# Performance work log

Hardware: AMD Instinct MI355X
Metric: run time of the kernel (lower is better)

## Reference

```python
import jax, jax.numpy as jnp
import numpy as np

N_NODES = 50000
N_EDGES = 1600000
IN_DIM = 128
HID = 128


def setup_inputs() -> dict:
    key = jax.random.key(0)
    ks = jax.random.split(key, 12)
    s = 1.0 / np.sqrt(HID)
    return {
        "x": jax.random.normal(ks[0], (N_NODES, IN_DIM), jnp.float32),
        "src": jax.random.randint(ks[1], (N_EDGES,), 0, N_NODES, jnp.int32),
        "dst": jax.random.randint(ks[2], (N_EDGES,), 0, N_NODES, jnp.int32),
        "W0": jax.random.normal(ks[3], (IN_DIM, HID), jnp.float32) * s,
        "b0": jnp.zeros((HID,), jnp.float32),
        "W1": jax.random.normal(ks[4], (HID, HID), jnp.float32) * s,
        "b1": jnp.zeros((HID,), jnp.float32),
        "W2": jax.random.normal(ks[5], (HID, HID), jnp.float32) * s,
        "b2": jnp.zeros((HID,), jnp.float32),
        "w_pg": jax.random.normal(ks[6], (HID, 1), jnp.float32) * s,
        "b_pg": jnp.zeros((1,), jnp.float32),
        "w_pd": jax.random.normal(ks[7], (HID, 1), jnp.float32) * s,
        "b_pd": jnp.zeros((1,), jnp.float32),
        "w_v": jax.random.normal(ks[8], (HID, 1), jnp.float32) * s,
        "b_v": jnp.zeros((1,), jnp.float32),
    }


def _gcn_layer(h, src, dst, W, b):
    # DGL-style GCN: gather source features along edges, sum-scatter to dst,
    # then per-node Linear + ReLU.  agg: [N, d]
    agg = jax.ops.segment_sum(h[src], dst, num_segments=N_NODES)
    return jax.nn.relu(agg @ W + b)


def reference(x, src, dst, W0, b0, W1, b1, W2, b2, w_pg, b_pg, w_pd, b_pd, w_v, b_v):
    h = _gcn_layer(x, src, dst, W0, b0)
    h = _gcn_layer(h, src, dst, W1, b1)
    h = _gcn_layer(h, src, dst, W2, b2)
    mN = jnp.mean(h, axis=0, keepdims=True)          # dgl.mean_nodes -> [1, HID]
    v = mN @ w_v + b_v                                # [1, 1]
    pi_graph = h @ w_pg + b_pg                        # [N, 1]
    pi_done = mN @ w_pd + b_pd                        # [1, 1]
    pi = jnp.concatenate([pi_graph, pi_done], axis=0)  # [N+1, 1]
    return (pi, v)
```

## Files before the change

kernel.cpp:

```cpp
#include <hip/hip_runtime.h>
#include <hip/hip_bf16.h>


#define HID 128
#define NBLK 256
#define BSH 6
#define SCAN_CHUNK 1024

typedef __attribute__((ext_vector_type(8))) short short8;
typedef __attribute__((ext_vector_type(4))) float f32x4;

__device__ __forceinline__ unsigned int f2bf(float f) {
    unsigned int u = __float_as_uint(f);
    return (u + 0x7fffu + ((u >> 16) & 1u)) >> 16;
}
__device__ __forceinline__ float bf2f(unsigned short u) {
    return __uint_as_float(((unsigned int)u) << 16);
}

__global__ __launch_bounds__(256) void f32_to_bf16_kernel(
        const float4* __restrict__ in, ushort4* __restrict__ out, int n4) {
    for (int i = blockIdx.x * blockDim.x + threadIdx.x; i < n4; i += gridDim.x * blockDim.x) {
        float4 v = in[i];
        ushort4 o;
        o.x = (unsigned short)f2bf(v.x); o.y = (unsigned short)f2bf(v.y);
        o.z = (unsigned short)f2bf(v.z); o.w = (unsigned short)f2bf(v.w);
        out[i] = o;
    }
}

__global__ __launch_bounds__(256) void pack_w3_kernel(
        const float* __restrict__ W0, const float* __restrict__ W1,
        const float* __restrict__ W2, unsigned short* __restrict__ pw) {
    for (int j = blockIdx.x * blockDim.x + threadIdx.x; j < 3 * 16384;
         j += gridDim.x * blockDim.x) {
        int jj = j & 16383, which = j >> 14;
        const float* W = (which == 0) ? W0 : (which == 1) ? W1 : W2;
        int i = jj & 7, lane = (jj >> 3) & 63, kk = (jj >> 9) & 3, c = (jj >> 11) & 7;
        int k = kk * 32 + (lane >> 4) * 8 + i;
        int col = c * 16 + (lane & 15);
        pw[j] = (unsigned short)f2bf(W[k * 128 + col]);
    }
}

__global__ __launch_bounds__(256) void bhist_kernel(const int* __restrict__ dst,
        int* __restrict__ tbl, int ne, int nb, int epb) {
    __shared__ int lcnt[1024];
    const int k = blockIdx.x, t = threadIdx.x;
    for (int b = t; b < nb; b += 256) lcnt[b] = 0;
    __syncthreads();
    const int beg = k * epb, end = min(ne, beg + epb);
    for (int j = beg + t; j < end; j += 256)
        atomicAdd(&lcnt[dst[j] >> BSH], 1);
    __syncthreads();
    for (int b = t; b < nb; b += 256) tbl[b * NBLK + k] = lcnt[b];
}

__global__ __launch_bounds__(256) void scan_p1_kernel(const int* __restrict__ tbl,
        int* __restrict__ bsum, int sz) {
    __shared__ int sh[256];
    const int g = blockIdx.x, t = threadIdx.x;
    const int base = g * SCAN_CHUNK + t * 4;
    int s = 0;
    if (base + 3 < sz) {
        int4 v = *(const int4*)(tbl + base);
        s = v.x + v.y + v.z + v.w;
    } else {
        for (int i = 0; i < 4; ++i) if (base + i < sz) s += tbl[base + i];
    }
    sh[t] = s;
    __syncthreads();
    for (int off = 128; off > 0; off >>= 1) {
        if (t < off) sh[t] += sh[t + off];
        __syncthreads();
    }
    if (t == 0) bsum[g] = sh[0];
}

__global__ __launch_bounds__(256) void scan_p2_kernel(int* __restrict__ bsum, int ng) {
    __shared__ int sh[256];
    const int t = threadIdx.x;
    int v = (t < ng) ? bsum[t] : 0;
    sh[t] = v;
    __syncthreads();
    for (int off = 1; off < 256; off <<= 1) {
        int a = sh[t];
        int b = (t >= off) ? sh[t - off] : 0;
        __syncthreads();
        sh[t] = a + b;
        __syncthreads();
    }
    if (t < ng) bsum[t] = sh[t] - v;
}

__global__ __launch_bounds__(256) void scan_p3_kernel(int* __restrict__ tbl,
        const int* __restrict__ bsum, int sz) {
    __shared__ int sh[256];
    const int g = blockIdx.x, t = threadIdx.x;
    const int base = g * SCAN_CHUNK + t * 4;
    int4 v = make_int4(0, 0, 0, 0);
    if (base + 3 < sz) {
        v = *(const int4*)(tbl + base);
    } else {
        if (base + 0 < sz) v.x = tbl[base + 0];
        if (base + 1 < sz) v.y = tbl[base + 1];
        if (base + 2 < sz) v.z = tbl[base + 2];
    }
    int s = v.x + v.y + v.z + v.w;
    sh[t] = s;
    __syncthreads();
    for (int off = 1; off < 256; off <<= 1) {
        int a = sh[t];
        int b = (t >= off) ? sh[t - off] : 0;
        __syncthreads();
        sh[t] = a + b;
        __syncthreads();
    }
    int pre = bsum[g] + sh[t] - s;
    int o0 = pre, o1 = pre + v.x, o2 = o1 + v.y, o3 = o2 + v.z;
    if (base + 3 < sz) {
        *(int4*)(tbl + base) = make_int4(o0, o1, o2, o3);
    } else {
        if (base + 0 < sz) tbl[base + 0] = o0;
        if (base + 1 < sz) tbl[base + 1] = o1;
        if (base + 2 < sz) tbl[base + 2] = o2;
    }
}

__global__ __launch_bounds__(256) void bucket_scatter_kernel(
        const int* __restrict__ src, const int* __restrict__ dst,
        const int* __restrict__ tbl, int* __restrict__ pairs,
        int ne, int nb, int epb) {
    __shared__ int cur[1024];
    const int k = blockIdx.x, t = threadIdx.x;
    for (int b = t; b < nb; b += 256) cur[b] = tbl[b * NBLK + k];
    __syncthreads();
    const int beg = k * epb, end = min(ne, beg + epb);
    for (int j = beg + t; j < end; j += 256) {
        int d = dst[j];
        int pos = atomicAdd(&cur[d >> BSH], 1);
        pairs[pos] = (src[j] << BSH) | (d & 63);
    }
}

__global__ __launch_bounds__(256) void fine_scatter_kernel(
        const int* __restrict__ pairs, const int* __restrict__ tbl,
        int* __restrict__ row_ptr, int* __restrict__ eidx,
        int ne, int nb, int n) {
    __shared__ int cnt[64], cur[64];
    const int b = blockIdx.x, t = threadIdx.x;
    const int node0 = b << BSH;
    if (t < 64) cnt[t] = 0;
    __syncthreads();
    const int beg = tbl[b * NBLK];
    const int end = (b == nb - 1) ? ne : tbl[(b + 1) * NBLK];
    for (int j = beg + t; j < end; j += 256) atomicAdd(&cnt[pairs[j] & 63], 1);
    __syncthreads();
    if (t == 0) {
        int run = beg;
        #pragma unroll
        for (int i = 0; i < 64; ++i) { cur[i] = run; run += cnt[i]; }
    }
    __syncthreads();
    if (t < 64 && node0 + t < n) row_ptr[node0 + t] = cur[t];
    if (b == nb - 1 && t == 0) row_ptr[n] = ne;
    __syncthreads();
    for (int j = beg + t; j < end; j += 256) {
        int v = pairs[j];
        int pos = atomicAdd(&cur[v & 63], 1);
        eidx[pos] = v >> BSH;
    }
}

__global__ __launch_bounds__(256) void layer_fused_kernel(
        const uint2* __restrict__ xb, const int* __restrict__ row_ptr,
        const int* __restrict__ eidx, const short* __restrict__ packw,
        const float* __restrict__ bias, unsigned short* __restrict__ hb,
        float* __restrict__ part, float* __restrict__ pig_out,
        const float* __restrict__ w_pg, const float* __restrict__ b_pg,
        int n) {
    __shared__ unsigned short Ash[64][136];
    __shared__ float colp[4][128];
    const int t = threadIdx.x;

    {
        const int grp = t >> 5, lane = t & 31;
        for (int i = 0; i < 8; ++i) {
            const int r = grp * 8 + i;
            const int g = blockIdx.x * 64 + r;
            float4 acc = make_float4(0.f, 0.f, 0.f, 0.f);
            if (g < n) {
                const int beg = row_ptr[g], end = row_ptr[g + 1];
                int e = beg;
                for (; e + 4 <= end; e += 4) {
                    int s0 = eidx[e], s1 = eidx[e + 1], s2 = eidx[e + 2], s3 = eidx[e + 3];
                    uint2 v0 = xb[(size_t)s0 * 32 + lane];
                    uint2 v1 = xb[(size_t)s1 * 32 + lane];
                    uint2 v2 = xb[(size_t)s2 * 32 + lane];
                    uint2 v3 = xb[(size_t)s3 * 32 + lane];
                    acc.x += __uint_as_float(v0.x << 16); acc.y += __uint_as_float(v0.x & 0xffff0000u);
                    acc.z += __uint_as_float(v0.y << 16); acc.w += __uint_as_float(v0.y & 0xffff0000u);
                    acc.x += __uint_as_float(v1.x << 16); acc.y += __uint_as_float(v1.x & 0xffff0000u);
                    acc.z += __uint_as_float(v1.y << 16); acc.w += __uint_as_float(v1.y & 0xffff0000u);
                    acc.x += __uint_as_float(v2.x << 16); acc.y += __uint_as_float(v2.x & 0xffff0000u);
                    acc.z += __uint_as_float(v2.y << 16); acc.w += __uint_as_float(v2.y & 0xffff0000u);
                    acc.x += __uint_as_float(v3.x << 16); acc.y += __uint_as_float(v3.x & 0xffff0000u);
                    acc.z += __uint_as_float(v3.y << 16); acc.w += __uint_as_float(v3.y & 0xffff0000u);
                }
                for (; e < end; ++e) {
                    int s = eidx[e];
                    uint2 v = xb[(size_t)s * 32 + lane];
                    acc.x += __uint_as_float(v.x << 16); acc.y += __uint_as_float(v.x & 0xffff0000u);
                    acc.z += __uint_as_float(v.y << 16); acc.w += __uint_as_float(v.y & 0xffff0000u);
                }
            }
            uint2 o;
            o.x = f2bf(acc.x) | (f2bf(acc.y) << 16);
            o.y = f2bf(acc.z) | (f2bf(acc.w) << 16);
            *(uint2*)&Ash[r][lane * 4] = o;
        }
    }
    __syncthreads();

    const int w = t >> 6, l = t & 63;
    const int m = l & 15, hi = l >> 4;
    const int row0 = blockIdx.x * 64 + w * 16;

    short8 afrag[4];
    #pragma unroll
    for (int kk = 0; kk < 4; ++kk)
        afrag[kk] = *(const short8*)&Ash[w * 16 + m][kk * 32 + hi * 8];

    f32x4 acc[8] = {};
    #pragma unroll
    for (int kk = 0; kk < 4; ++kk) {
        #pragma unroll
        for (int c = 0; c < 8; ++c) {
            short8 bfrag = *(const short8*)(packw + ((size_t)(c * 4 + kk) * 64 + l) * 8);
            acc[c] = __builtin_amdgcn_mfma_f32_16x16x32_bf16(afrag[kk], bfrag, acc[c], 0, 0, 0);
        }
    }

    float hvv[8][4];
    #pragma unroll
    for (int c = 0; c < 8; ++c) {
        float bcol = bias[c * 16 + m];
        #pragma unroll
        for (int r = 0; r < 4; ++r) {
            int row = row0 + hi * 4 + r;
            float hv = (row < n) ? fmaxf(acc[c][r] + bcol, 0.f) : 0.f;
            hvv[c][r] = hv;
            if (row < n)
                hb[(size_t)row * 128 + c * 16 + m] = (unsigned short)f2bf(hv);
        }
    }

    if (w_pg) {
        #pragma unroll
        for (int r = 0; r < 4; ++r) {
            float p = 0.f;
            #pragma unroll
            for (int c = 0; c < 8; ++c) p += hvv[c][r] * w_pg[c * 16 + m];
            #pragma unroll
            for (int off = 1; off < 16; off <<= 1) p += __shfl_xor(p, off);
            int row = row0 + hi * 4 + r;
            if (m == 0 && row < n) pig_out[row] = p + b_pg[0];
        }
        #pragma unroll
        for (int c = 0; c < 8; ++c) {
            float v = hvv[c][0] + hvv[c][1] + hvv[c][2] + hvv[c][3];
            v += __shfl_xor(v, 16);
            v += __shfl_xor(v, 32);
            if (hi == 0) colp[w][c * 16 + m] = v;
        }
        __syncthreads();
        if (t < 128)
            part[(size_t)blockIdx.x * 128 + t] =
                colp[0][t] + colp[1][t] + colp[2][t] + colp[3][t];
    }
}

__global__ __launch_bounds__(1024) void head_final_kernel(
        const float* __restrict__ part, int nparts,
        const float* __restrict__ w_v, const float* __restrict__ b_v,
        const float* __restrict__ w_pd, const float* __restrict__ b_pd,
        float* __restrict__ out, int n_nodes) {
    __shared__ float sh[32][128];
    __shared__ float sv[128], sd[128];
    const int t = threadIdx.x;
    const int d4 = t & 31, pg = t >> 5;
    float4 acc = make_float4(0.f, 0.f, 0.f, 0.f);
    for (int i = pg; i < nparts; i += 32) {
        float4 v = *(const float4*)(part + (size_t)i * 128 + d4 * 4);
        acc.x += v.x; acc.y += v.y; acc.z += v.z; acc.w += v.w;
    }
    *(float4*)&sh[pg][d4 * 4] = acc;
    __syncthreads();
    for (int off = 16; off > 0; off >>= 1) {
        if (pg < off) {
            float4 a = *(float4*)&sh[pg][d4 * 4];
            float4 b = *(float4*)&sh[pg + off][d4 * 4];
            a.x += b.x; a.y += b.y; a.z += b.z; a.w += b.w;
            *(float4*)&sh[pg][d4 * 4] = a;
        }
        __syncthreads();
    }
    if (t < 128) {
        float mm = sh[0][t] / (float)n_nodes;
        sv[t] = mm * w_v[t];
        sd[t] = mm * w_pd[t];
    }
    __syncthreads();
    for (int off = 64; off > 0; off >>= 1) {
        if (t < off) { sv[t] += sv[t + off]; sd[t] += sd[t + off]; }
        __syncthreads();
    }
    if (t == 0) {
        out[n_nodes] = sd[0] + b_pd[0];
        out[n_nodes + 1] = sv[0] + b_v[0];
    }
}

static inline size_t align_up(size_t v, size_t a) { return (v + a - 1) & ~(a - 1); }

extern "C" void kernel_launch(void* const* d_in, const int* in_sizes, int n_in,
                              void* d_out, int out_size, void* d_ws, size_t ws_size,
                              hipStream_t stream) {
    const float* x    = (const float*)d_in[0];
    const int*   src  = (const int*)d_in[1];
    const int*   dst  = (const int*)d_in[2];
    const float* W0   = (const float*)d_in[3];
    const float* b0   = (const float*)d_in[4];
    const float* W1   = (const float*)d_in[5];
    const float* b1   = (const float*)d_in[6];
    const float* W2   = (const float*)d_in[7];
    const float* b2   = (const float*)d_in[8];
    const float* w_pg = (const float*)d_in[9];
    const float* b_pg = (const float*)d_in[10];
    const float* w_pd = (const float*)d_in[11];
    const float* b_pd = (const float*)d_in[12];
    const float* w_v  = (const float*)d_in[13];
    const float* b_v  = (const float*)d_in[14];
    float* out = (float*)d_out;

    const int NN = in_sizes[0] / HID;
    const int NE = in_sizes[1];
    const int NB = (NN + 63) >> BSH;
    const int SZ = NB * NBLK;
    const int EPB = (NE + NBLK - 1) / NBLK;
    const int NG = (SZ + SCAN_CHUNK - 1) / SCAN_CHUNK;
    const int LBLK = (NN + 63) / 64;

    char* w = (char*)d_ws;
    int* tbl      = (int*)w;            w += align_up((size_t)SZ * 4, 256);
    int* bsum     = (int*)w;            w += align_up((size_t)256 * 4, 256);
    int* row_ptr  = (int*)w;            w += align_up((size_t)(NN + 1) * 4, 256);
    int* eidx     = (int*)w;            w += align_up((size_t)NE * 4, 256);
    unsigned short* xb = (unsigned short*)w; w += align_up((size_t)NN * HID * 2, 256);
    unsigned short* hb = (unsigned short*)w; w += align_up((size_t)NN * HID * 2, 256);
    unsigned short* hb2 = (unsigned short*)w; w += align_up((size_t)NN * HID * 2, 256);
    unsigned short* pw = (unsigned short*)w; w += align_up((size_t)3 * 16384 * 2, 256);
    float* part   = (float*)w;          w += align_up((size_t)LBLK * 128 * 4, 256);
    int* pairs    = (int*)hb;
    (void)ws_size; (void)n_in; (void)out_size;

    f32_to_bf16_kernel<<<2048, 256, 0, stream>>>((const float4*)x, (ushort4*)xb, NN * 32);
    pack_w3_kernel<<<48, 256, 0, stream>>>(W0, W1, W2, pw);

    bhist_kernel<<<NBLK, 256, 0, stream>>>(dst, tbl, NE, NB, EPB);
    scan_p1_kernel<<<NG, 256, 0, stream>>>(tbl, bsum, SZ);
    scan_p2_kernel<<<1, 256, 0, stream>>>(bsum, NG);
    scan_p3_kernel<<<NG, 256, 0, stream>>>(tbl, bsum, SZ);
    bucket_scatter_kernel<<<NBLK, 256, 0, stream>>>(src, dst, tbl, pairs, NE, NB, EPB);
    fine_scatter_kernel<<<NB, 256, 0, stream>>>(pairs, tbl, row_ptr, eidx, NE, NB, NN);

    layer_fused_kernel<<<LBLK, 256, 0, stream>>>(
        (const uint2*)xb, row_ptr, eidx, (const short*)pw, b0, hb2,
        nullptr, nullptr, nullptr, nullptr, NN);
    layer_fused_kernel<<<LBLK, 256, 0, stream>>>(
        (const uint2*)hb2, row_ptr, eidx, (const short*)(pw + 16384), b1, hb,
        nullptr, nullptr, nullptr, nullptr, NN);
    layer_fused_kernel<<<LBLK, 256, 0, stream>>>(
        (const uint2*)hb, row_ptr, eidx, (const short*)(pw + 32768), b2, hb2,
        part, out, w_pg, b_pg, NN);

    head_final_kernel<<<1, 1024, 0, stream>>>(part, LBLK, w_v, b_v, w_pd, b_pd, out, NN);
}
```

Measured before the change: 314.4 us.

## Split fused aggregate+GEMM layer into separate aggregation and MFMA GEMM kernels

Unfuses each GCN layer into a standalone gather/aggregate kernel, with one 32-lane group per node and an 8-way unrolled edge loop, followed by a separate MFMA GEMM kernel that reads the aggregated bf16 rows from global memory. The aim is more parallelism and memory-level parallelism in the gather, which was limited by each block serially processing 64 rows before its GEMM. The cost is an extra global write and read of the N×128 bf16 aggregate per layer and three more kernel launches. The buffers are also rearranged so aggb is reused across layers and hb is overwritten in place by the GEMM output.

```diff
diff --git a/kernel.cpp b/kernel.cpp
--- a/kernel.cpp
+++ b/kernel.cpp
@@ -172,64 +172,80 @@
     }
 }
 
-__global__ __launch_bounds__(256) void layer_fused_kernel(
+__global__ __launch_bounds__(256) void aggregate_bf_kernel(
         const uint2* __restrict__ xb, const int* __restrict__ row_ptr,
-        const int* __restrict__ eidx, const short* __restrict__ packw,
-        const float* __restrict__ bias, unsigned short* __restrict__ hb,
+        const int* __restrict__ eidx, uint2* __restrict__ aggb, int n) {
+    int g = (int)((blockIdx.x * blockDim.x + threadIdx.x) >> 5);
+    int lane = threadIdx.x & 31;
+    if (g >= n) return;
+    const int beg = row_ptr[g], end = row_ptr[g + 1];
+    float4 acc = make_float4(0.f, 0.f, 0.f, 0.f);
+    int e = beg;
+    for (; e + 8 <= end; e += 8) {
+        uint2 v0 = xb[(size_t)eidx[e + 0] * 32 + lane];
+        uint2 v1 = xb[(size_t)eidx[e + 1] * 32 + lane];
+        uint2 v2 = xb[(size_t)eidx[e + 2] * 32 + lane];
+        uint2 v3 = xb[(size_t)eidx[e + 3] * 32 + lane];
+        uint2 v4 = xb[(size_t)eidx[e + 4] * 32 + lane];
+        uint2 v5 = xb[(size_t)eidx[e + 5] * 32 + lane];
+        uint2 v6 = xb[(size_t)eidx[e + 6] * 32 + lane];
+        uint2 v7 = xb[(size_t)eidx[e + 7] * 32 + lane];
+        acc.x += __uint_as_float(v0.x << 16); acc.y += __uint_as_float(v0.x & 0xffff0000u);
+        acc.z += __uint_as_float(v0.y << 16); acc.w += __uint_as_float(v0.y & 0xffff0000u);
+        acc.x += __uint_as_float(v1.x << 16); acc.y += __uint_as_float(v1.x & 0xffff0000u);
+        acc.z += __uint_as_float(v1.y << 16); acc.w += __uint_as_float(v1.y & 0xffff0000u);
+        acc.x += __uint_as_float(v2.x << 16); acc.y += __uint_as_float(v2.x & 0xffff0000u);
+        acc.z += __uint_as_float(v2.y << 16); acc.w += __uint_as_float(v2.y & 0xffff0000u);
+        acc.x += __uint_as_float(v3.x << 16); acc.y += __uint_as_float(v3.x & 0xffff0000u);
+        acc.z += __uint_as_float(v3.y << 16); acc.w += __uint_as_float(v3.y & 0xffff0000u);
+        acc.x += __uint_as_float(v4.x << 16); acc.y += __uint_as_float(v4.x & 0xffff0000u);
+        acc.z += __uint_as_float(v4.y << 16); acc.w += __uint_as_float(v4.y & 0xffff0000u);
+        acc.x += __uint_as_float(v5.x << 16); acc.y += __uint_as_float(v5.x & 0xffff0000u);
+        acc.z += __uint_as_float(v5.y << 16); acc.w += __uint_as_float(v5.y & 0xffff0000u);
+        acc.x += __uint_as_float(v6.x << 16); acc.y += __uint_as_float(v6.x & 0xffff0000u);
+        acc.z += __uint_as_float(v6.y << 16); acc.w += __uint_as_float(v6.y & 0xffff0000u);
+        acc.x += __uint_as_float(v7.x << 16); acc.y += __uint_as_float(v7.x & 0xffff0000u);
+        acc.z += __uint_as_float(v7.y << 16); acc.w += __uint_as_float(v7.y & 0xffff0000u);
+    }
+    for (; e + 2 <= end; e += 2) {
+        uint2 v0 = xb[(size_t)eidx[e + 0] * 32 + lane];
+        uint2 v1 = xb[(size_t)eidx[e + 1] * 32 + lane];
+        acc.x += __uint_as_float(v0.x << 16); acc.y += __uint_as_float(v0.x & 0xffff0000u);
+        acc.z += __uint_as_float(v0.y << 16); acc.w += __uint_as_float(v0.y & 0xffff0000u);
+        acc.x += __uint_as_float(v1.x << 16); acc.y += __uint_as_float(v1.x & 0xffff0000u);
+        acc.z += __uint_as_float(v1.y << 16); acc.w += __uint_as_float(v1.y & 0xffff0000u);
+    }
+    if (e < end) {
+        uint2 v = xb[(size_t)eidx[e] * 32 + lane];
+        acc.x += __uint_as_float(v.x << 16); acc.y += __uint_as_float(v.x & 0xffff0000u);
+        acc.z += __uint_as_float(v.y << 16); acc.w += __uint_as_float(v.y & 0xffff0000u);
+    }
+    uint2 o;
+    o.x = f2bf(acc.x) | (f2bf(acc.y) << 16);
+    o.y = f2bf(acc.z) | (f2bf(acc.w) << 16);
+    aggb[(size_t)g * 32 + lane] = o;
+}
+
+__global__ __launch_bounds__(256) void gemm_mfma_kernel(
+        const short* __restrict__ A, const short* __restrict__ packw,
+        const float* __restrict__ bias, unsigned short* __restrict__ out, int M,
         float* __restrict__ part, float* __restrict__ pig_out,
-        const float* __restrict__ w_pg, const float* __restrict__ b_pg,
-        int n) {
-    __shared__ unsigned short Ash[64][136];
+        const float* __restrict__ w_pg, const float* __restrict__ b_pg) {
     __shared__ float colp[4][128];
-    const int t = threadIdx.x;
-
-    {
-        const int grp = t >> 5, lane = t & 31;
-        for (int i = 0; i < 8; ++i) {
-            const int r = grp * 8 + i;
-            const int g = blockIdx.x * 64 + r;
-            float4 acc = make_float4(0.f, 0.f, 0.f, 0.f);
-            if (g < n) {
-                const int beg = row_ptr[g], end = row_ptr[g + 1];
-                int e = beg;
-                for (; e + 4 <= end; e += 4) {
-                    int s0 = eidx[e], s1 = eidx[e + 1], s2 = eidx[e + 2], s3 = eidx[e + 3];
-                    uint2 v0 = xb[(size_t)s0 * 32 + lane];
-                    uint2 v1 = xb[(size_t)s1 * 32 + lane];
-                    uint2 v2 = xb[(size_t)s2 * 32 + lane];
-                    uint2 v3 = xb[(size_t)s3 * 32 + lane];
-                    acc.x += __uint_as_float(v0.x << 16); acc.y += __uint_as_float(v0.x & 0xffff0000u);
-                    acc.z += __uint_as_float(v0.y << 16); acc.w += __uint_as_float(v0.y & 0xffff0000u);
-                    acc.x += __uint_as_float(v1.x << 16); acc.y += __uint_as_float(v1.x & 0xffff0000u);
-                    acc.z += __uint_as_float(v1.y << 16); acc.w += __uint_as_float(v1.y & 0xffff0000u);
-                    acc.x += __uint_as_float(v2.x << 16); acc.y += __uint_as_float(v2.x & 0xffff0000u);
-                    acc.z += __uint_as_float(v2.y << 16); acc.w += __uint_as_float(v2.y & 0xffff0000u);
-                    acc.x += __uint_as_float(v3.x << 16); acc.y += __uint_as_float(v3.x & 0xffff0000u);
-                    acc.z += __uint_as_float(v3.y << 16); acc.w += __uint_as_float(v3.y & 0xffff0000u);
-                }
-                for (; e < end; ++e) {
-                    int s = eidx[e];
-                    uint2 v = xb[(size_t)s * 32 + lane];
-                    acc.x += __uint_as_float(v.x << 16); acc.y += __uint_as_float(v.x & 0xffff0000u);
-                    acc.z += __uint_as_float(v.y << 16); acc.w += __uint_as_float(v.y & 0xffff0000u);
-                }
-            }
-            uint2 o;
-            o.x = f2bf(acc.x) | (f2bf(acc.y) << 16);
-            o.y = f2bf(acc.z) | (f2bf(acc.w) << 16);
-            *(uint2*)&Ash[r][lane * 4] = o;
-        }
-    }
-    __syncthreads();
-
-    const int w = t >> 6, l = t & 63;
+    const int w = threadIdx.x >> 6, l = threadIdx.x & 63;
     const int m = l & 15, hi = l >> 4;
     const int row0 = blockIdx.x * 64 + w * 16;
+    const int arow = row0 + m;
+    const bool valid = arow < M;
 
     short8 afrag[4];
     #pragma unroll
-    for (int kk = 0; kk < 4; ++kk)
-        afrag[kk] = *(const short8*)&Ash[w * 16 + m][kk * 32 + hi * 8];
+    for (int kk = 0; kk < 4; ++kk) {
+        if (valid)
+            afrag[kk] = *(const short8*)(A + (size_t)arow * 128 + kk * 32 + hi * 8);
+        else
+            afrag[kk] = short8{0, 0, 0, 0, 0, 0, 0, 0};
+    }
 
     f32x4 acc[8] = {};
     #pragma unroll
@@ -248,10 +264,10 @@
         #pragma unroll
         for (int r = 0; r < 4; ++r) {
             int row = row0 + hi * 4 + r;
-            float hv = (row < n) ? fmaxf(acc[c][r] + bcol, 0.f) : 0.f;
+            float hv = (row < M) ? fmaxf(acc[c][r] + bcol, 0.f) : 0.f;
             hvv[c][r] = hv;
-            if (row < n)
-                hb[(size_t)row * 128 + c * 16 + m] = (unsigned short)f2bf(hv);
+            if (row < M)
+                out[(size_t)row * 128 + c * 16 + m] = (unsigned short)f2bf(hv);
         }
     }
 
@@ -264,7 +280,7 @@
             #pragma unroll
             for (int off = 1; off < 16; off <<= 1) p += __shfl_xor(p, off);
             int row = row0 + hi * 4 + r;
-            if (m == 0 && row < n) pig_out[row] = p + b_pg[0];
+            if (m == 0 && row < M) pig_out[row] = p + b_pg[0];
         }
         #pragma unroll
         for (int c = 0; c < 8; ++c) {
@@ -274,6 +290,7 @@
             if (hi == 0) colp[w][c * 16 + m] = v;
         }
         __syncthreads();
+        const int t = threadIdx.x;
         if (t < 128)
             part[(size_t)blockIdx.x * 128 + t] =
                 colp[0][t] + colp[1][t] + colp[2][t] + colp[3][t];
@@ -349,19 +366,19 @@
     const int SZ = NB * NBLK;
     const int EPB = (NE + NBLK - 1) / NBLK;
     const int NG = (SZ + SCAN_CHUNK - 1) / SCAN_CHUNK;
-    const int LBLK = (NN + 63) / 64;
+    const int GBLK = (NN + 63) / 64;
 
     char* w = (char*)d_ws;
     int* tbl      = (int*)w;            w += align_up((size_t)SZ * 4, 256);
     int* bsum     = (int*)w;            w += align_up((size_t)256 * 4, 256);
     int* row_ptr  = (int*)w;            w += align_up((size_t)(NN + 1) * 4, 256);
     int* eidx     = (int*)w;            w += align_up((size_t)NE * 4, 256);
-    unsigned short* xb = (unsigned short*)w; w += align_up((size_t)NN * HID * 2, 256);
-    unsigned short* hb = (unsigned short*)w; w += align_up((size_t)NN * HID * 2, 256);
-    unsigned short* hb2 = (unsigned short*)w; w += align_up((size_t)NN * HID * 2, 256);
-    unsigned short* pw = (unsigned short*)w; w += align_up((size_t)3 * 16384 * 2, 256);
-    float* part   = (float*)w;          w += align_up((size_t)LBLK * 128 * 4, 256);
-    int* pairs    = (int*)hb;
+    unsigned short* xb   = (unsigned short*)w; w += align_up((size_t)NN * HID * 2, 256);
+    unsigned short* aggb = (unsigned short*)w; w += align_up((size_t)NN * HID * 2, 256);
+    unsigned short* hb   = (unsigned short*)w; w += align_up((size_t)NN * HID * 2, 256);
+    unsigned short* pw   = (unsigned short*)w; w += align_up((size_t)3 * 16384 * 2, 256);
+    float* part   = (float*)w;          w += align_up((size_t)GBLK * 128 * 4, 256);
+    int* pairs    = (int*)aggb;
     (void)ws_size; (void)n_in; (void)out_size;
 
     f32_to_bf16_kernel<<<2048, 256, 0, stream>>>((const float4*)x, (ushort4*)xb, NN * 32);
@@ -374,15 +391,20 @@
     bucket_scatter_kernel<<<NBLK, 256, 0, stream>>>(src, dst, tbl, pairs, NE, NB, EPB);
     fine_scatter_kernel<<<NB, 256, 0, stream>>>(pairs, tbl, row_ptr, eidx, NE, NB, NN);
 
-    layer_fused_kernel<<<LBLK, 256, 0, stream>>>(
-        (const uint2*)xb, row_ptr, eidx, (const short*)pw, b0, hb2,
-        nullptr, nullptr, nullptr, nullptr, NN);
-    layer_fused_kernel<<<LBLK, 256, 0, stream>>>(
-        (const uint2*)hb2, row_ptr, eidx, (const short*)(pw + 16384), b1, hb,
-        nullptr, nullptr, nullptr, nullptr, NN);
-    layer_fused_kernel<<<LBLK, 256, 0, stream>>>(
-        (const uint2*)hb, row_ptr, eidx, (const short*)(pw + 32768), b2, hb2,
-        part, out, w_pg, b_pg, NN);
-
-    head_final_kernel<<<1, 1024, 0, stream>>>(part, LBLK, w_v, b_v, w_pd, b_pd, out, NN);
-}
+    const int agg_blocks = (NN * 32 + 255) / 256;
+
+    aggregate_bf_kernel<<<agg_blocks, 256, 0, stream>>>((const uint2*)xb, row_ptr, eidx,
+                                                        (uint2*)aggb, NN);
+    gemm_mfma_kernel<<<GBLK, 256, 0, stream>>>((const short*)aggb, (const short*)pw,
+                                               b0, hb, NN, nullptr, nullptr, nullptr, nullptr);
+    aggregate_bf_kernel<<<agg_blocks, 256, 0, stream>>>((const uint2*)hb, row_ptr, eidx,
+                                                        (uint2*)aggb, NN);
+    gemm_mfma_kernel<<<GBLK, 256, 0, stream>>>((const short*)aggb, (const short*)(pw + 16384),
+                                               b1, hb, NN, nullptr, nullptr, nullptr, nullptr);
+    aggregate_bf_kernel<<<agg_blocks, 256, 0, stream>>>((const uint2*)hb, row_ptr, eidx,
+                                                        (uint2*)aggb, NN);
+    gemm_mfma_kernel<<<GBLK, 256, 0, stream>>>((const short*)aggb, (const short*)(pw + 32768),
+                                               b2, hb, NN, part, out, w_pg, b_pg);
+
+    head_final_kernel<<<1, 1024, 0, stream>>>(part, GBLK, w_v, b_v, w_pd, b_pd, out, NN);
+}
```

New measurement: 267.7 us. -14.9%, faster.
